# Performance work log

Hardware: AMD Instinct MI355X
Metric: run time of the kernel (lower is better)

Reference implementation:

```python
import jax, jax.numpy as jnp
import numpy as np

MAX_SEQ = 2048
NUM_HEADS = 32
NUM_KV_HEADS = 4
HEAD_DIM = 256
HIDDEN = 4096
ROTARY_DIM = 64  # head_dim * partial_rotary_factor(0.25)
THETA = 10000000.0
EPS = 1e-6
GROUPS = NUM_HEADS // NUM_KV_HEADS
SCALE = 1.0 / np.sqrt(HEAD_DIM)


def rms_norm(x, w):
    xf = x.astype(jnp.float32)
    norm = jax.lax.rsqrt(jnp.mean(xf * xf, axis=-1, keepdims=True) + EPS)
    return (xf * norm * w).astype(x.dtype)


def partial_rope(x, position):
    # x: [B, H, 1, D]; rotate first ROTARY_DIM dims (split-half convention)
    half = ROTARY_DIM // 2
    inv_freq = 1.0 / (THETA ** (jnp.arange(half, dtype=jnp.float32) / half))
    freqs = position.astype(jnp.float32) * inv_freq  # [half]
    cos = jnp.cos(freqs).reshape(1, 1, 1, -1)
    sin = jnp.sin(freqs).reshape(1, 1, 1, -1)
    x1 = x[..., :half]
    x2 = x[..., half:ROTARY_DIM]
    x_pass = x[..., ROTARY_DIM:]
    rot = jnp.concatenate([x1 * cos - x2 * sin, x2 * cos + x1 * sin], axis=-1)
    return jnp.concatenate([rot, x_pass], axis=-1)


def setup_inputs() -> dict:
    key = jax.random.key(0)
    ks = jax.random.split(key, 10)
    pos = 1500
    position = jnp.array([pos], dtype=jnp.int32)
    idx = jnp.arange(MAX_SEQ)
    mask = jnp.where(idx <= pos, 0.0, -1e9).astype(jnp.float32).reshape(1, 1, 1, MAX_SEQ)
    onehot = (idx == pos).astype(jnp.float32).reshape(1, 1, MAX_SEQ, 1)
    return {
        "x": jax.random.normal(ks[0], (1, 1, HIDDEN), dtype=jnp.float32),
        "position": position,
        "mask": mask,
        "k_cache": jax.random.normal(ks[1], (1, NUM_KV_HEADS, MAX_SEQ, HEAD_DIM), dtype=jnp.float32),
        "v_cache": jax.random.normal(ks[2], (1, NUM_KV_HEADS, MAX_SEQ, HEAD_DIM), dtype=jnp.float32),
        "onehot": onehot,
        "q_proj_w": jax.random.normal(ks[3], (2 * NUM_HEADS * HEAD_DIM, HIDDEN), dtype=jnp.float32) * 0.02,
        "k_proj_w": jax.random.normal(ks[4], (NUM_KV_HEADS * HEAD_DIM, HIDDEN), dtype=jnp.float32) * 0.02,
        "v_proj_w": jax.random.normal(ks[5], (NUM_KV_HEADS * HEAD_DIM, HIDDEN), dtype=jnp.float32) * 0.02,
        "o_proj_w": jax.random.normal(ks[6], (HIDDEN, NUM_HEADS * HEAD_DIM), dtype=jnp.float32) * 0.02,
        "q_norm_w": jnp.ones((HEAD_DIM,), dtype=jnp.float32),
        "k_norm_w": jnp.ones((HEAD_DIM,), dtype=jnp.float32),
    }


def reference(x, position, mask, k_cache, v_cache, onehot,
              q_proj_w, k_proj_w, v_proj_w, o_proj_w, q_norm_w, k_norm_w):
    B, T, _ = x.shape  # B=T=1
    # Q + gate interleaved per head
    qg = jnp.einsum('bth,oh->bto', x, q_proj_w).reshape(B, T, NUM_HEADS, 2 * HEAD_DIM)
    q = qg[..., :HEAD_DIM]                      # [B,T,H,D]
    gate = qg[..., HEAD_DIM:].reshape(B, T, -1)  # [B,T,H*D]
    q = jnp.transpose(q, (0, 2, 1, 3))           # [B,H,T,D]
    k = jnp.einsum('bth,oh->bto', x, k_proj_w).reshape(B, T, NUM_KV_HEADS, HEAD_DIM).transpose(0, 2, 1, 3)
    v = jnp.einsum('bth,oh->bto', x, v_proj_w).reshape(B, T, NUM_KV_HEADS, HEAD_DIM).transpose(0, 2, 1, 3)
    q = rms_norm(q, q_norm_w)
    k = rms_norm(k, k_norm_w)
    q = partial_rope(q, position)
    k = partial_rope(k, position)
    # full-buffer onehot cache update (same math as mul_/add_)
    k_cache = k_cache * (1.0 - onehot) + k * onehot  # [B,KV,S,D]
    v_cache = v_cache * (1.0 - onehot) + v * onehot
    # GQA: group query heads over kv heads without materializing expanded KV
    qg_heads = q.reshape(B, NUM_KV_HEADS, GROUPS, T, HEAD_DIM)
    attn = jnp.einsum('bgktd,bgsd->bgkts', qg_heads, k_cache) * SCALE  # [B,KV,G,T,S]
    attn = attn + mask[:, :, None]  # mask [B,1,1,T,S] broadcast
    attn = jax.nn.softmax(attn, axis=-1)
    out = jnp.einsum('bgkts,bgsd->bgktd', attn, v_cache)  # [B,KV,G,T,D]
    out = out.reshape(B, NUM_HEADS, T, HEAD_DIM).transpose(0, 2, 1, 3).reshape(B, T, -1)
    out = out * jax.nn.sigmoid(gate)
    return jnp.einsum('bto,ho->bth', out, o_proj_w)
```

## Files before the change

kernel.cpp:

```cpp
#include <hip/hip_runtime.h>
#include <math.h>

#define MAX_SEQ   2048
#define NUM_HEADS 32
#define NUM_KV    4
#define HEAD_DIM  256
#define HIDDEN    4096
#define ROT_DIM   64
#define GROUPS    8
#define SCALE     0.0625f
#define CHUNK     32
#define NCHUNK    (MAX_SEQ / CHUNK)

typedef float f4 __attribute__((ext_vector_type(4)));

__device__ inline f4 ld4(const float* p) {
    return *reinterpret_cast<const f4*>(p);
}

__global__ __launch_bounds__(256) void gemv_qkv(
    const float* __restrict__ x,
    const float* __restrict__ qw,
    const float* __restrict__ kw,
    const float* __restrict__ vw,
    const int*   __restrict__ posp,
    float* __restrict__ out,
    float* __restrict__ tab)
{
    if (blockIdx.x == 4608) {
        const int i = threadIdx.x;
        if (i < 32) {
            const double inv_freq = pow(10000000.0, -(double)i / 32.0);
            const double ang = (double)posp[0] * inv_freq;
            tab[i]      = (float)cos(ang);
            tab[i + 32] = (float)sin(ang);
        }
        return;
    }
    const int wave = threadIdx.x >> 6;
    const int lane = threadIdx.x & 63;
    const int row  = blockIdx.x * 4 + wave;

    const float* w;
    if (row < 16384)      w = qw + (size_t)row * HIDDEN;
    else if (row < 17408) w = kw + (size_t)(row - 16384) * HIDDEN;
    else                  w = vw + (size_t)(row - 17408) * HIDDEN;

    float acc = 0.f;
#pragma unroll
    for (int it = 0; it < HIDDEN / 256; ++it) {
        const int idx = it * 256 + lane * 4;
        f4 wv = ld4(w + idx);
        f4 xv = ld4(x + idx);
        acc += wv[0] * xv[0] + wv[1] * xv[1] + wv[2] * xv[2] + wv[3] * xv[3];
    }
#pragma unroll
    for (int off = 32; off >= 1; off >>= 1) acc += __shfl_xor(acc, off);
    if (lane == 0) out[row] = acc;
}

__global__ __launch_bounds__(256) void attn_partial(
    const float* __restrict__ qkv,
    const float* __restrict__ qnw,
    const float* __restrict__ knw,
    const float* __restrict__ kcache,
    const float* __restrict__ vcache,
    const float* __restrict__ tab,
    const int*   __restrict__ posp,
    float* __restrict__ part_m,
    float* __restrict__ part_l,
    float* __restrict__ part_acc)
{
    const int kv  = blockIdx.x;
    const int c   = blockIdx.y;
    const int pos = posp[0];
    const int s0  = c * CHUNK;
    const int tid = threadIdx.x;

    if (s0 > pos) {
        if (tid == 0) {
#pragma unroll
            for (int g = 0; g < GROUPS; ++g) {
                const int pid = (kv * GROUPS + g) * NCHUNK + c;
                part_m[pid] = -1e30f; part_l[pid] = 0.f;
            }
        }
        return;
    }
    const int s1 = min(s0 + CHUNK, pos + 1);

    const int lane = tid & 63;
    const int wave = tid >> 6;
    const int d    = tid;

    const float* kbase = kcache + (size_t)kv * MAX_SEQ * HEAD_DIM;
    const float* vbase = vcache + (size_t)kv * MAX_SEQ * HEAD_DIM;

    float vals[9];
#pragma unroll
    for (int g = 0; g < GROUPS; ++g)
        vals[g] = qkv[(kv * GROUPS + g) * 512 + d];
    vals[8] = qkv[16384 + kv * HEAD_DIM + d];
    const float vnew_d = qkv[17408 + kv * HEAD_DIM + d];

    float vpre[CHUNK];
#pragma unroll
    for (int u = 0; u < CHUNK; ++u) {
        const int s = s0 + u;
        const int srow = (s < pos) ? s : 0;
        vpre[u] = vbase[(size_t)srow * HEAD_DIM + d];
    }

    const int i0 = wave * 8;
    f4 kpre[8];
#pragma unroll
    for (int j = 0; j < 8; ++j) {
        const int s = s0 + i0 + j;
        const int srow = (s < pos) ? s : 0;
        kpre[j] = ld4(kbase + (size_t)srow * HEAD_DIM + lane * 4);
    }

    __shared__ float ssred[9][4];
    {
        float sq[9];
#pragma unroll
        for (int g = 0; g < 9; ++g) sq[g] = vals[g] * vals[g];
#pragma unroll
        for (int off = 32; off >= 1; off >>= 1) {
#pragma unroll
            for (int g = 0; g < 9; ++g) sq[g] += __shfl_xor(sq[g], off);
        }
        if (lane == 0) {
#pragma unroll
            for (int g = 0; g < 9; ++g) ssred[g][wave] = sq[g];
        }
    }
    __syncthreads();

    __shared__ __align__(16) float qn[9][HEAD_DIM];
    {
        const float qw_ = qnw[d];
        const float kw_ = knw[d];
#pragma unroll
        for (int g = 0; g < 9; ++g) {
            const float tot  = ssred[g][0] + ssred[g][1] + ssred[g][2] + ssred[g][3];
            const float norm = rsqrtf(tot * (1.0f / HEAD_DIM) + 1e-6f);
            qn[g][d] = vals[g] * norm * (g < 8 ? qw_ : kw_);
        }
    }
    __syncthreads();

    {
        const bool rot = (d < ROT_DIM);
        const int  i   = d & 31;
        const float co = tab[i];
        const float si = tab[i + 32];
        float rv[9];
#pragma unroll
        for (int g = 0; g < 9; ++g) {
            const float x1 = qn[g][i];
            const float x2 = qn[g][i + 32];
            rv[g] = (d < 32) ? (x1 * co - x2 * si) : (x2 * co + x1 * si);
        }
        __syncthreads();
        if (rot) {
#pragma unroll
            for (int g = 0; g < 9; ++g) qn[g][d] = rv[g];
        }
        __syncthreads();
    }

#pragma unroll
    for (int u = 0; u < CHUNK; ++u)
        if (s0 + u >= pos) vpre[u] = vnew_d;
    const f4 kf4 = *reinterpret_cast<const f4*>(&qn[8][lane * 4]);
#pragma unroll
    for (int j = 0; j < 8; ++j)
        if (s0 + i0 + j >= pos) kpre[j] = kf4;

    f4 q8[GROUPS];
#pragma unroll
    for (int g = 0; g < GROUPS; ++g)
        q8[g] = *reinterpret_cast<const f4*>(&qn[g][lane * 4]);

    __shared__ float sc[GROUPS][CHUNK];
    __shared__ __align__(16) float pl[GROUPS][CHUNK];
    __shared__ float mh[GROUPS], lh[GROUPS];

#pragma unroll
    for (int j = 0; j < 8; ++j) {
        const int s = s0 + i0 + j;
        const bool valid = (s < s1);
        float part[GROUPS];
#pragma unroll
        for (int g = 0; g < GROUPS; ++g) {
            f4 t = q8[g] * kpre[j];
            part[g] = t[0] + t[1] + t[2] + t[3];
        }
#pragma unroll
        for (int off = 32; off >= 1; off >>= 1) {
#pragma unroll
            for (int g = 0; g < GROUPS; ++g)
                part[g] += __shfl_xor(part[g], off);
        }
        if (lane == 0) {
#pragma unroll
            for (int g = 0; g < GROUPS; ++g)
                sc[g][i0 + j] = valid ? part[g] * SCALE : -1e30f;
        }
    }
    __syncthreads();

    {
        const int h = tid >> 5;
        const int j = tid & 31;
        float v = sc[h][j];
        float m = v;
#pragma unroll
        for (int off = 16; off >= 1; off >>= 1)
            m = fmaxf(m, __shfl_xor(m, off));
        const float p = expf(v - m);
        pl[h][j] = p;
        float ls = p;
#pragma unroll
        for (int off = 16; off >= 1; off >>= 1)
            ls += __shfl_xor(ls, off);
        if (j == 0) { mh[h] = m; lh[h] = ls; }
    }
    __syncthreads();

    float acc[GROUPS];
#pragma unroll
    for (int g = 0; g < GROUPS; ++g) acc[g] = 0.f;
#pragma unroll
    for (int i4 = 0; i4 < CHUNK / 4; ++i4) {
        f4 p4[GROUPS];
#pragma unroll
        for (int g = 0; g < GROUPS; ++g)
            p4[g] = *reinterpret_cast<const f4*>(&pl[g][i4 * 4]);
#pragma unroll
        for (int u = 0; u < 4; ++u) {
#pragma unroll
            for (int g = 0; g < GROUPS; ++g)
                acc[g] += p4[g][u] * vpre[i4 * 4 + u];
        }
    }
#pragma unroll
    for (int g = 0; g < GROUPS; ++g) {
        const int pid = (kv * GROUPS + g) * NCHUNK + c;
        part_acc[(size_t)pid * HEAD_DIM + d] = acc[g];
        if (tid == 0) { part_m[pid] = mh[g]; part_l[pid] = lh[g]; }
    }
}

__global__ __launch_bounds__(256) void attn_combine(
    const float* __restrict__ part_m,
    const float* __restrict__ part_l,
    const float* __restrict__ part_acc,
    const float* __restrict__ qkv,
    float* __restrict__ attn_gated)
{
    const int h = blockIdx.x;
    const int d = threadIdx.x;

    float M = -1e30f;
#pragma unroll 8
    for (int c = 0; c < NCHUNK; ++c) M = fmaxf(M, part_m[h * NCHUNK + c]);

    float L = 0.f, acc = 0.f;
#pragma unroll 8
    for (int c = 0; c < NCHUNK; ++c) {
        const float w = expf(part_m[h * NCHUNK + c] - M);
        L   += part_l[h * NCHUNK + c] * w;
        acc += part_acc[(size_t)(h * NCHUNK + c) * HEAD_DIM + d] * w;
    }
    const float o   = acc / L;
    const float g   = qkv[h * 512 + 256 + d];
    const float sig = 1.0f / (1.0f + expf(-g));
    attn_gated[h * HEAD_DIM + d] = o * sig;
}

__global__ __launch_bounds__(256) void gemv_o(
    const float* __restrict__ vec,
    const float* __restrict__ w,
    float* __restrict__ out)
{
    const int wave = threadIdx.x >> 6;
    const int lane = threadIdx.x & 63;
    const int row  = blockIdx.x * 4 + wave;
    const float* wr = w + (size_t)row * 8192;

    float acc = 0.f;
#pragma unroll
    for (int it = 0; it < 8192 / 256; ++it) {
        const int idx = it * 256 + lane * 4;
        f4 wv = ld4(wr + idx);
        f4 xv = ld4(vec + idx);
        acc += wv[0] * xv[0] + wv[1] * xv[1] + wv[2] * xv[2] + wv[3] * xv[3];
    }
#pragma unroll
    for (int off = 32; off >= 1; off >>= 1) acc += __shfl_xor(acc, off);
    if (lane == 0) out[row] = acc;
}

extern "C" void kernel_launch(void* const* d_in, const int* in_sizes, int n_in,
                              void* d_out, int out_size, void* d_ws, size_t ws_size,
                              hipStream_t stream) {
    const float* x        = (const float*)d_in[0];
    const int*   position = (const int*)  d_in[1];
    const float* k_cache  = (const float*)d_in[3];
    const float* v_cache  = (const float*)d_in[4];
    const float* q_proj_w = (const float*)d_in[6];
    const float* k_proj_w = (const float*)d_in[7];
    const float* v_proj_w = (const float*)d_in[8];
    const float* o_proj_w = (const float*)d_in[9];
    const float* q_norm_w = (const float*)d_in[10];
    const float* k_norm_w = (const float*)d_in[11];
    float* out = (float*)d_out;

    float* ws         = (float*)d_ws;
    float* qkv        = ws;
    float* tab        = ws + 18432;
    float* part_m     = ws + 18496;
    float* part_l     = ws + 20544;
    float* part_acc   = ws + 22592;
    float* attn_gated = ws + 546880;

    gemv_qkv<<<4609, 256, 0, stream>>>(x, q_proj_w, k_proj_w, v_proj_w,
                                       position, qkv, tab);
    dim3 g2(NUM_KV, NCHUNK);
    attn_partial<<<g2, 256, 0, stream>>>(qkv, q_norm_w, k_norm_w,
                                         k_cache, v_cache, tab, position,
                                         part_m, part_l, part_acc);
    attn_combine<<<NUM_HEADS, 256, 0, stream>>>(part_m, part_l, part_acc, qkv,
                                                attn_gated);
    gemv_o<<<1024, 256, 0, stream>>>(attn_gated, o_proj_w, out);
}
```

Measured before the change: 100.5 us.

## Fuse attention combine into partial kernel via last-arriver atomic counter

Removes the separate attn_combine launch. Each attn_partial block increments a per-KV-head atomic counter after a threadfence, and the last eight blocks to arrive for each KV head spin until all chunks finish, then each merges one query head's partial softmax results and applies the sigmoid gate. The counter is reset inside gemv_qkv's extra block. This saves one kernel launch and its gap, but adds a spin-wait that relies on all 256 blocks being co-resident or finishing, plus atomic and fence overhead.

```diff
diff --git a/kernel.cpp b/kernel.cpp
--- a/kernel.cpp
+++ b/kernel.cpp
@@ -25,10 +25,12 @@
     const float* __restrict__ vw,
     const int*   __restrict__ posp,
     float* __restrict__ out,
-    float* __restrict__ tab)
+    float* __restrict__ tab,
+    int*   __restrict__ ctr)
 {
     if (blockIdx.x == 4608) {
         const int i = threadIdx.x;
+        if (i < NUM_KV) ctr[i] = 0;
         if (i < 32) {
             const double inv_freq = pow(10000000.0, -(double)i / 32.0);
             const double ang = (double)posp[0] * inv_freq;
@@ -69,7 +71,9 @@
     const int*   __restrict__ posp,
     float* __restrict__ part_m,
     float* __restrict__ part_l,
-    float* __restrict__ part_acc)
+    float* __restrict__ part_acc,
+    int*   __restrict__ ctr,
+    float* __restrict__ attn_gated)
 {
     const int kv  = blockIdx.x;
     const int c   = blockIdx.y;
@@ -77,7 +81,8 @@
     const int s0  = c * CHUNK;
     const int tid = threadIdx.x;
 
-    if (s0 > pos) {
+    const bool empty = (s0 > pos);
+    if (empty) {
         if (tid == 0) {
 #pragma unroll
             for (int g = 0; g < GROUPS; ++g) {
@@ -85,199 +90,207 @@
                 part_m[pid] = -1e30f; part_l[pid] = 0.f;
             }
         }
-        return;
-    }
-    const int s1 = min(s0 + CHUNK, pos + 1);
-
-    const int lane = tid & 63;
-    const int wave = tid >> 6;
-    const int d    = tid;
-
-    const float* kbase = kcache + (size_t)kv * MAX_SEQ * HEAD_DIM;
-    const float* vbase = vcache + (size_t)kv * MAX_SEQ * HEAD_DIM;
-
-    float vals[9];
-#pragma unroll
-    for (int g = 0; g < GROUPS; ++g)
-        vals[g] = qkv[(kv * GROUPS + g) * 512 + d];
-    vals[8] = qkv[16384 + kv * HEAD_DIM + d];
-    const float vnew_d = qkv[17408 + kv * HEAD_DIM + d];
-
-    float vpre[CHUNK];
-#pragma unroll
-    for (int u = 0; u < CHUNK; ++u) {
-        const int s = s0 + u;
-        const int srow = (s < pos) ? s : 0;
-        vpre[u] = vbase[(size_t)srow * HEAD_DIM + d];
-    }
-
-    const int i0 = wave * 8;
-    f4 kpre[8];
-#pragma unroll
-    for (int j = 0; j < 8; ++j) {
-        const int s = s0 + i0 + j;
-        const int srow = (s < pos) ? s : 0;
-        kpre[j] = ld4(kbase + (size_t)srow * HEAD_DIM + lane * 4);
-    }
-
-    __shared__ float ssred[9][4];
-    {
-        float sq[9];
-#pragma unroll
-        for (int g = 0; g < 9; ++g) sq[g] = vals[g] * vals[g];
-#pragma unroll
-        for (int off = 32; off >= 1; off >>= 1) {
-#pragma unroll
-            for (int g = 0; g < 9; ++g) sq[g] += __shfl_xor(sq[g], off);
-        }
-        if (lane == 0) {
-#pragma unroll
-            for (int g = 0; g < 9; ++g) ssred[g][wave] = sq[g];
-        }
-    }
+    } else {
+        const int s1 = min(s0 + CHUNK, pos + 1);
+
+        const int lane = tid & 63;
+        const int wave = tid >> 6;
+        const int d    = tid;
+
+        const float* kbase = kcache + (size_t)kv * MAX_SEQ * HEAD_DIM;
+        const float* vbase = vcache + (size_t)kv * MAX_SEQ * HEAD_DIM;
+
+        float vals[9];
+#pragma unroll
+        for (int g = 0; g < GROUPS; ++g)
+            vals[g] = qkv[(kv * GROUPS + g) * 512 + d];
+        vals[8] = qkv[16384 + kv * HEAD_DIM + d];
+        const float vnew_d = qkv[17408 + kv * HEAD_DIM + d];
+
+        float vpre[CHUNK];
+#pragma unroll
+        for (int u = 0; u < CHUNK; ++u) {
+            const int s = s0 + u;
+            const int srow = (s < pos) ? s : 0;
+            vpre[u] = vbase[(size_t)srow * HEAD_DIM + d];
+        }
+
+        const int i0 = wave * 8;
+        f4 kpre[8];
+#pragma unroll
+        for (int j = 0; j < 8; ++j) {
+            const int s = s0 + i0 + j;
+            const int srow = (s < pos) ? s : 0;
+            kpre[j] = ld4(kbase + (size_t)srow * HEAD_DIM + lane * 4);
+        }
+
+        __shared__ float ssred[9][4];
+        {
+            float sq[9];
+#pragma unroll
+            for (int g = 0; g < 9; ++g) sq[g] = vals[g] * vals[g];
+#pragma unroll
+            for (int off = 32; off >= 1; off >>= 1) {
+#pragma unroll
+                for (int g = 0; g < 9; ++g) sq[g] += __shfl_xor(sq[g], off);
+            }
+            if (lane == 0) {
+#pragma unroll
+                for (int g = 0; g < 9; ++g) ssred[g][wave] = sq[g];
+            }
+        }
+        __syncthreads();
+
+        __shared__ __align__(16) float qn[9][HEAD_DIM];
+        {
+            const float qw_ = qnw[d];
+            const float kw_ = knw[d];
+#pragma unroll
+            for (int g = 0; g < 9; ++g) {
+                const float tot  = ssred[g][0] + ssred[g][1] + ssred[g][2] + ssred[g][3];
+                const float norm = rsqrtf(tot * (1.0f / HEAD_DIM) + 1e-6f);
+                qn[g][d] = vals[g] * norm * (g < 8 ? qw_ : kw_);
+            }
+        }
+        __syncthreads();
+
+        {
+            const bool rot = (d < ROT_DIM);
+            const int  i   = d & 31;
+            const float co = tab[i];
+            const float si = tab[i + 32];
+            float rv[9];
+#pragma unroll
+            for (int g = 0; g < 9; ++g) {
+                const float x1 = qn[g][i];
+                const float x2 = qn[g][i + 32];
+                rv[g] = (d < 32) ? (x1 * co - x2 * si) : (x2 * co + x1 * si);
+            }
+            __syncthreads();
+            if (rot) {
+#pragma unroll
+                for (int g = 0; g < 9; ++g) qn[g][d] = rv[g];
+            }
+            __syncthreads();
+        }
+
+#pragma unroll
+        for (int u = 0; u < CHUNK; ++u)
+            if (s0 + u >= pos) vpre[u] = vnew_d;
+        const f4 kf4 = *reinterpret_cast<const f4*>(&qn[8][lane * 4]);
+#pragma unroll
+        for (int j = 0; j < 8; ++j)
+            if (s0 + i0 + j >= pos) kpre[j] = kf4;
+
+        f4 q8[GROUPS];
+#pragma unroll
+        for (int g = 0; g < GROUPS; ++g)
+            q8[g] = *reinterpret_cast<const f4*>(&qn[g][lane * 4]);
+
+        __shared__ float sc[GROUPS][CHUNK];
+        __shared__ __align__(16) float pl[GROUPS][CHUNK];
+        __shared__ float mh[GROUPS], lh[GROUPS];
+
+#pragma unroll
+        for (int j = 0; j < 8; ++j) {
+            const int s = s0 + i0 + j;
+            const bool valid = (s < s1);
+            float part[GROUPS];
+#pragma unroll
+            for (int g = 0; g < GROUPS; ++g) {
+                f4 t = q8[g] * kpre[j];
+                part[g] = t[0] + t[1] + t[2] + t[3];
+            }
+#pragma unroll
+            for (int off = 32; off >= 1; off >>= 1) {
+#pragma unroll
+                for (int g = 0; g < GROUPS; ++g)
+                    part[g] += __shfl_xor(part[g], off);
+            }
+            if (lane == 0) {
+#pragma unroll
+                for (int g = 0; g < GROUPS; ++g)
+                    sc[g][i0 + j] = valid ? part[g] * SCALE : -1e30f;
+            }
+        }
+        __syncthreads();
+
+        {
+            const int h = tid >> 5;
+            const int j = tid & 31;
+            float v = sc[h][j];
+            float m = v;
+#pragma unroll
+            for (int off = 16; off >= 1; off >>= 1)
+                m = fmaxf(m, __shfl_xor(m, off));
+            const float p = expf(v - m);
+            pl[h][j] = p;
+            float ls = p;
+#pragma unroll
+            for (int off = 16; off >= 1; off >>= 1)
+                ls += __shfl_xor(ls, off);
+            if (j == 0) { mh[h] = m; lh[h] = ls; }
+        }
+        __syncthreads();
+
+        float acc[GROUPS];
+#pragma unroll
+        for (int g = 0; g < GROUPS; ++g) acc[g] = 0.f;
+#pragma unroll
+        for (int i4 = 0; i4 < CHUNK / 4; ++i4) {
+            f4 p4[GROUPS];
+#pragma unroll
+            for (int g = 0; g < GROUPS; ++g)
+                p4[g] = *reinterpret_cast<const f4*>(&pl[g][i4 * 4]);
+#pragma unroll
+            for (int u = 0; u < 4; ++u) {
+#pragma unroll
+                for (int g = 0; g < GROUPS; ++g)
+                    acc[g] += p4[g][u] * vpre[i4 * 4 + u];
+            }
+        }
+#pragma unroll
+        for (int g = 0; g < GROUPS; ++g) {
+            const int pid = (kv * GROUPS + g) * NCHUNK + c;
+            part_acc[(size_t)pid * HEAD_DIM + d] = acc[g];
+            if (tid == 0) { part_m[pid] = mh[g]; part_l[pid] = lh[g]; }
+        }
+    }
+
+    __threadfence();
+    __shared__ int ord_s;
+    if (tid == 0) ord_s = atomicAdd(&ctr[kv], 1);
     __syncthreads();
-
-    __shared__ __align__(16) float qn[9][HEAD_DIM];
-    {
-        const float qw_ = qnw[d];
-        const float kw_ = knw[d];
-#pragma unroll
-        for (int g = 0; g < 9; ++g) {
-            const float tot  = ssred[g][0] + ssred[g][1] + ssred[g][2] + ssred[g][3];
-            const float norm = rsqrtf(tot * (1.0f / HEAD_DIM) + 1e-6f);
-            qn[g][d] = vals[g] * norm * (g < 8 ? qw_ : kw_);
-        }
+    const int ord = ord_s;
+    if (ord < NCHUNK - 8) return;
+
+    const int g  = ord - (NCHUNK - 8);
+    const int hh = kv * GROUPS + g;
+
+    if (tid == 0) {
+        while (__hip_atomic_load(&ctr[kv], __ATOMIC_ACQUIRE,
+                                 __HIP_MEMORY_SCOPE_AGENT) < NCHUNK) { }
     }
     __syncthreads();
-
-    {
-        const bool rot = (d < ROT_DIM);
-        const int  i   = d & 31;
-        const float co = tab[i];
-        const float si = tab[i + 32];
-        float rv[9];
-#pragma unroll
-        for (int g = 0; g < 9; ++g) {
-            const float x1 = qn[g][i];
-            const float x2 = qn[g][i + 32];
-            rv[g] = (d < 32) ? (x1 * co - x2 * si) : (x2 * co + x1 * si);
-        }
-        __syncthreads();
-        if (rot) {
-#pragma unroll
-            for (int g = 0; g < 9; ++g) qn[g][d] = rv[g];
-        }
-        __syncthreads();
-    }
-
-#pragma unroll
-    for (int u = 0; u < CHUNK; ++u)
-        if (s0 + u >= pos) vpre[u] = vnew_d;
-    const f4 kf4 = *reinterpret_cast<const f4*>(&qn[8][lane * 4]);
-#pragma unroll
-    for (int j = 0; j < 8; ++j)
-        if (s0 + i0 + j >= pos) kpre[j] = kf4;
-
-    f4 q8[GROUPS];
-#pragma unroll
-    for (int g = 0; g < GROUPS; ++g)
-        q8[g] = *reinterpret_cast<const f4*>(&qn[g][lane * 4]);
-
-    __shared__ float sc[GROUPS][CHUNK];
-    __shared__ __align__(16) float pl[GROUPS][CHUNK];
-    __shared__ float mh[GROUPS], lh[GROUPS];
-
-#pragma unroll
-    for (int j = 0; j < 8; ++j) {
-        const int s = s0 + i0 + j;
-        const bool valid = (s < s1);
-        float part[GROUPS];
-#pragma unroll
-        for (int g = 0; g < GROUPS; ++g) {
-            f4 t = q8[g] * kpre[j];
-            part[g] = t[0] + t[1] + t[2] + t[3];
-        }
-#pragma unroll
-        for (int off = 32; off >= 1; off >>= 1) {
-#pragma unroll
-            for (int g = 0; g < GROUPS; ++g)
-                part[g] += __shfl_xor(part[g], off);
-        }
-        if (lane == 0) {
-#pragma unroll
-            for (int g = 0; g < GROUPS; ++g)
-                sc[g][i0 + j] = valid ? part[g] * SCALE : -1e30f;
-        }
-    }
-    __syncthreads();
-
-    {
-        const int h = tid >> 5;
-        const int j = tid & 31;
-        float v = sc[h][j];
-        float m = v;
-#pragma unroll
-        for (int off = 16; off >= 1; off >>= 1)
-            m = fmaxf(m, __shfl_xor(m, off));
-        const float p = expf(v - m);
-        pl[h][j] = p;
-        float ls = p;
-#pragma unroll
-        for (int off = 16; off >= 1; off >>= 1)
-            ls += __shfl_xor(ls, off);
-        if (j == 0) { mh[h] = m; lh[h] = ls; }
-    }
-    __syncthreads();
-
-    float acc[GROUPS];
-#pragma unroll
-    for (int g = 0; g < GROUPS; ++g) acc[g] = 0.f;
-#pragma unroll
-    for (int i4 = 0; i4 < CHUNK / 4; ++i4) {
-        f4 p4[GROUPS];
-#pragma unroll
-        for (int g = 0; g < GROUPS; ++g)
-            p4[g] = *reinterpret_cast<const f4*>(&pl[g][i4 * 4]);
-#pragma unroll
-        for (int u = 0; u < 4; ++u) {
-#pragma unroll
-            for (int g = 0; g < GROUPS; ++g)
-                acc[g] += p4[g][u] * vpre[i4 * 4 + u];
-        }
-    }
-#pragma unroll
-    for (int g = 0; g < GROUPS; ++g) {
-        const int pid = (kv * GROUPS + g) * NCHUNK + c;
-        part_acc[(size_t)pid * HEAD_DIM + d] = acc[g];
-        if (tid == 0) { part_m[pid] = mh[g]; part_l[pid] = lh[g]; }
-    }
-}
-
-__global__ __launch_bounds__(256) void attn_combine(
-    const float* __restrict__ part_m,
-    const float* __restrict__ part_l,
-    const float* __restrict__ part_acc,
-    const float* __restrict__ qkv,
-    float* __restrict__ attn_gated)
-{
-    const int h = blockIdx.x;
-    const int d = threadIdx.x;
-
+    __threadfence();
+
+    const int d = tid;
     float M = -1e30f;
 #pragma unroll 8
-    for (int c = 0; c < NCHUNK; ++c) M = fmaxf(M, part_m[h * NCHUNK + c]);
-
-    float L = 0.f, acc = 0.f;
+    for (int c2 = 0; c2 < NCHUNK; ++c2)
+        M = fmaxf(M, part_m[hh * NCHUNK + c2]);
+
+    float L = 0.f, acc2 = 0.f;
 #pragma unroll 8
-    for (int c = 0; c < NCHUNK; ++c) {
-        const float w = expf(part_m[h * NCHUNK + c] - M);
-        L   += part_l[h * NCHUNK + c] * w;
-        acc += part_acc[(size_t)(h * NCHUNK + c) * HEAD_DIM + d] * w;
-    }
-    const float o   = acc / L;
-    const float g   = qkv[h * 512 + 256 + d];
-    const float sig = 1.0f / (1.0f + expf(-g));
-    attn_gated[h * HEAD_DIM + d] = o * sig;
+    for (int c2 = 0; c2 < NCHUNK; ++c2) {
+        const float w = expf(part_m[hh * NCHUNK + c2] - M);
+        L    += part_l[hh * NCHUNK + c2] * w;
+        acc2 += part_acc[(size_t)(hh * NCHUNK + c2) * HEAD_DIM + d] * w;
+    }
+    const float o    = acc2 / L;
+    const float gate = qkv[hh * 512 + 256 + d];
+    const float sig  = 1.0f / (1.0f + expf(-gate));
+    attn_gated[hh * HEAD_DIM + d] = o * sig;
 }
 
 __global__ __launch_bounds__(256) void gemv_o(
@@ -321,18 +334,18 @@
     float* ws         = (float*)d_ws;
     float* qkv        = ws;
     float* tab        = ws + 18432;
-    float* part_m     = ws + 18496;
-    float* part_l     = ws + 20544;
-    float* part_acc   = ws + 22592;
-    float* attn_gated = ws + 546880;
+    int*   ctr        = (int*)(ws + 18496);
+    float* part_m     = ws + 18560;
+    float* part_l     = ws + 20608;
+    float* part_acc   = ws + 22656;
+    float* attn_gated = ws + 546944;
 
     gemv_qkv<<<4609, 256, 0, stream>>>(x, q_proj_w, k_proj_w, v_proj_w,
-                                       position, qkv, tab);
+                                       position, qkv, tab, ctr);
     dim3 g2(NUM_KV, NCHUNK);
     attn_partial<<<g2, 256, 0, stream>>>(qkv, q_norm_w, k_norm_w,
                                          k_cache, v_cache, tab, position,
-                                         part_m, part_l, part_acc);
-    attn_combine<<<NUM_HEADS, 256, 0, stream>>>(part_m, part_l, part_acc, qkv,
-                                                attn_gated);
+                                         part_m, part_l, part_acc,
+                                         ctr, attn_gated);
     gemv_o<<<1024, 256, 0, stream>>>(attn_gated, o_proj_w, out);
 }
```

Result: slower. 131.5 us (+30.8%).
